# Optimization experiments

Measured on AMD Instinct MI355X. Metric: run time of the kernel, lower is better.

The kernel has to match this reference:

```python
import jax, jax.numpy as jnp
import numpy as np

N = 50000      # nodes
E = 800000     # edges (avg degree 16)
D = 64         # num_node_features
H = 64         # hidden_channels
G = 512        # graphs in batch
OUT = 32       # final linear output
NEG_SLOPE = 0.2


def setup_inputs() -> dict:
    key = jax.random.key(0)
    ks = jax.random.split(key, 20)
    s = 0.1  # param init scale
    inp = {
        "x": jax.random.normal(ks[0], (N, D), jnp.float32),
        "edge_index": jax.random.randint(ks[1], (2, E), 0, N, dtype=jnp.int64),
        "batch": jnp.sort(jax.random.randint(ks[2], (N,), 0, G, dtype=jnp.int64)),
        # GATv2 layer 1 (D -> H)
        "Wl1": jax.random.normal(ks[3], (D, H), jnp.float32) * s,
        "bl1": jnp.zeros((H,), jnp.float32),
        "Wr1": jax.random.normal(ks[4], (D, H), jnp.float32) * s,
        "br1": jnp.zeros((H,), jnp.float32),
        "att1": jax.random.normal(ks[5], (H,), jnp.float32) * s,
        "bias1": jnp.zeros((H,), jnp.float32),
        # GATv2 layer 2 (H -> H)
        "Wl2": jax.random.normal(ks[6], (H, H), jnp.float32) * s,
        "bl2": jnp.zeros((H,), jnp.float32),
        "Wr2": jax.random.normal(ks[7], (H, H), jnp.float32) * s,
        "br2": jnp.zeros((H,), jnp.float32),
        "att2": jax.random.normal(ks[8], (H,), jnp.float32) * s,
        "bias2": jnp.zeros((H,), jnp.float32),
        # final classifier
        "lin_w": jax.random.normal(ks[9], (H, OUT), jnp.float32) * s,
        "lin_b": jnp.zeros((OUT,), jnp.float32),
    }
    return inp


def _gatv2(x, src, dst, Wl, bl, Wr, br, att, bias):
    # GATv2Conv, heads=1, PyG semantics: messages flow src -> dst
    xl = x @ Wl + bl                       # [N, H] source transform (also the message)
    xr = x @ Wr + br                       # [N, H] destination transform
    z = xl[src] + xr[dst]                  # [E, H] gather
    e = jax.nn.leaky_relu(z, NEG_SLOPE) @ att  # [E] edge scores
    # segment softmax over edges grouped by destination node
    m = jax.ops.segment_max(e, dst, num_segments=N)   # [N]
    ex = jnp.exp(e - m[dst])                          # [E]
    denom = jax.ops.segment_sum(ex, dst, num_segments=N)  # [N]
    alpha = ex / denom[dst]                            # [E]
    out = jax.ops.segment_sum(alpha[:, None] * xl[src], dst, num_segments=N)  # [N, H]
    return out + bias


def reference(x, edge_index, batch,
              Wl1, bl1, Wr1, br1, att1, bias1,
              Wl2, bl2, Wr2, br2, att2, bias2,
              lin_w, lin_b):
    src, dst = edge_index[0], edge_index[1]
    h = jax.nn.relu(_gatv2(x, src, dst, Wl1, bl1, Wr1, br1, att1, bias1))
    h = jax.nn.relu(_gatv2(h, src, dst, Wl2, bl2, Wr2, br2, att2, bias2))
    # global mean pool over graphs
    sums = jax.ops.segment_sum(h, batch, num_segments=G)          # [G, H]
    cnts = jax.ops.segment_sum(jnp.ones((h.shape[0],), h.dtype), batch, num_segments=G)
    pooled = sums / jnp.maximum(cnts, 1.0)[:, None]
    # dropout(p=0.5) is identity at inference
    return pooled @ lin_w + lin_b                                  # [G, 32]
```

## Files before the change

kernel.cpp:

```cpp
#include <hip/hip_runtime.h>
#include <hip/hip_fp16.h>
#include <math.h>


#define ELLC    48
#define OVF_CAP 65536
#define ECHUNK  2048

typedef int      vint4 __attribute__((ext_vector_type(4)));
typedef _Float16 half4 __attribute__((ext_vector_type(4)));

#define GROWS 32
template <typename T>
__device__ __forceinline__ void dual_gemm_slim(
    int bid, int t,
    const T* __restrict__ X,
    const float* __restrict__ Wl, const float* __restrict__ bl,
    const float* __restrict__ Wr, const float* __restrict__ br,
    _Float16* __restrict__ xl, float* __restrict__ xr, int n,
    float* xS) {
    int row0 = bid * GROWS;
    for (int i = t; i < GROWS * 16; i += 256) {
        int r = row0 + (i >> 4);
        float4 v = make_float4(0.f, 0.f, 0.f, 0.f);
        if (r < n) {
            if constexpr (sizeof(T) == 2) {
                half4 hv = ((const half4*)(X + (size_t)r * 64))[i & 15];
                v = make_float4((float)hv[0], (float)hv[1], (float)hv[2], (float)hv[3]);
            } else {
                v = ((const float4*)(X + (size_t)r * 64))[i & 15];
            }
        }
        ((float4*)xS)[i] = v;
    }
    __syncthreads();
    int h  = t & 63;
    int rb = t >> 6;
    float accl[8], accr[8];
#pragma unroll
    for (int i = 0; i < 8; ++i) { accl[i] = 0.f; accr[i] = 0.f; }
#pragma unroll 4
    for (int d = 0; d < 64; ++d) {
        float wl = Wl[d * 64 + h];
        float wr = Wr[d * 64 + h];
#pragma unroll
        for (int i = 0; i < 8; ++i) {
            float xv = xS[(rb + 4 * i) * 64 + d];
            accl[i] += xv * wl;
            accr[i] += xv * wr;
        }
    }
    float blv = bl[h], brv = br[h];
#pragma unroll
    for (int i = 0; i < 8; ++i) {
        int r = row0 + rb + 4 * i;
        if (r < n) {
            xl[(size_t)r * 64 + h] = (_Float16)(accl[i] + blv);
            xr[(size_t)r * 64 + h] = accr[i] + brv;
        }
    }
}

__global__ __launch_bounds__(256) void dual_gemm64_f16_kernel(
    const _Float16* __restrict__ X,
    const float* __restrict__ Wl, const float* __restrict__ bl,
    const float* __restrict__ Wr, const float* __restrict__ br,
    _Float16* __restrict__ xl, float* __restrict__ xr, int n) {
    __shared__ float xS[GROWS * 64];
    dual_gemm_slim<_Float16>(blockIdx.x, threadIdx.x, X, Wl, bl, Wr, br,
                             xl, xr, n, xS);
}

__global__ __launch_bounds__(256) void fill_gemm_kernel(
    const int* __restrict__ src, const int* __restrict__ dst,
    int* __restrict__ cnt, unsigned short* __restrict__ ell,
    int* __restrict__ novf, int* __restrict__ ovf_dst, int* __restrict__ ovf_src,
    int E, int N, int psize, int fb, int ggrid,
    const float* __restrict__ X,
    const float* __restrict__ Wl, const float* __restrict__ bl,
    const float* __restrict__ Wr, const float* __restrict__ br,
    _Float16* __restrict__ xl, float* __restrict__ xr) {
    __shared__ float xS[GROWS * 64];
    int b = blockIdx.x;
    int q = b / 24, r = b % 24;
    if (r >= 16) {
        int vg = q * 8 + (r - 16);
        if (vg < ggrid)
            dual_gemm_slim<float>(vg, threadIdx.x, X, Wl, bl, Wr, br,
                                  xl, xr, N, xS);
        return;
    }
    int vb = q * 16 + r;
    if (vb >= fb) return;
    int t     = threadIdx.x;
    int chunk = vb >> 3;
    int p     = vb & 7;
    int d0    = p * psize;
    int d1    = min(N, d0 + psize);
    int e0    = chunk * ECHUNK;
    int e1    = min(E, e0 + ECHUNK);
    int nq    = (e1 - e0) >> 2;
    const vint4* dst4 = (const vint4*)(dst + e0);
    const vint4* src4 = (const vint4*)(src + e0);

    auto scatter4 = [&](vint4 dv, vint4 sv) {
#pragma unroll
        for (int k = 0; k < 4; ++k) {
            int d = dv[k];
            int s = sv[k];
            if (d >= d0 && d < d1) {
                int pos = atomicAdd(&cnt[d], 1);
                if (pos < ELLC) {
                    ell[d * ELLC + pos] = (unsigned short)s;
                } else {
                    int j = atomicAdd(novf, 1);
                    if (j < OVF_CAP) { ovf_dst[j] = d; ovf_src[j] = s; }
                }
            }
        }
    };

    if (nq == (ECHUNK >> 2)) {
        vint4 dvA = __builtin_nontemporal_load(&dst4[t]);
        vint4 svA = __builtin_nontemporal_load(&src4[t]);
        vint4 dvB = __builtin_nontemporal_load(&dst4[t + 256]);
        vint4 svB = __builtin_nontemporal_load(&src4[t + 256]);
        scatter4(dvA, svA);
        scatter4(dvB, svB);
    } else {
        for (int qq = t; qq < nq; qq += 256) {
            vint4 dv = __builtin_nontemporal_load(&dst4[qq]);
            vint4 sv = __builtin_nontemporal_load(&src4[qq]);
            scatter4(dv, sv);
        }
        for (int e = e0 + (nq << 2) + t; e < e1; e += 256) {
            int d = dst[e];
            if (d >= d0 && d < d1) {
                int pos = atomicAdd(&cnt[d], 1);
                int s   = src[e];
                if (pos < ELLC) {
                    ell[d * ELLC + pos] = (unsigned short)s;
                } else {
                    int j = atomicAdd(novf, 1);
                    if (j < OVF_CAP) { ovf_dst[j] = d; ovf_src[j] = s; }
                }
            }
        }
    }
}

__global__ __launch_bounds__(256) void gat_aggregate_kernel(
    const _Float16* __restrict__ xl, const float* __restrict__ xr,
    const int* __restrict__ cnt, const unsigned short* __restrict__ ell,
    const int* __restrict__ novf, const int* __restrict__ ovf_dst,
    const int* __restrict__ ovf_src,
    const float* __restrict__ att, const float* __restrict__ bias,
    _Float16* __restrict__ out, int n) {
    int wid  = (blockIdx.x * blockDim.x + threadIdx.x) >> 6;
    int lane = threadIdx.x & 63;
    if (wid >= n) return;
    int g = lane >> 4;
    int l = lane & 15;
    int d = wid;

    float4 att4 = ((const float4*)att)[l];
    float4 b4   = ((const float4*)bias)[l];
    int deg_d = cnt[d];
    int nd  = min(deg_d, ELLC);
    int beg = d * ELLC;

    float  s   = 0.f;
    float4 acc = make_float4(0.f, 0.f, 0.f, 0.f);

    if (deg_d > 0) {
        int myidx = 0;
        if (lane < ELLC) myidx = (int)ell[beg + lane];
        int i_first = __shfl(myidx, 0);

        float4 xr4 = ((const float4*)(xr + (size_t)d * 64))[l];

#pragma unroll 6
        for (int k = 0; k * 8 < nd; ++k) {
            int  sa = k * 8 + g, sb = sa + 4;
            bool aa = sa < nd,   ab = sb < nd;
            int  i0 = __shfl(myidx, sa); if (!aa) i0 = i_first;
            int  i1 = __shfl(myidx, sb); if (!ab) i1 = i_first;
            half4 h0 = ((const half4*)(xl + (size_t)i0 * 64))[l];
            half4 h1 = ((const half4*)(xl + (size_t)i1 * 64))[l];
            float4 x0 = make_float4((float)h0[0], (float)h0[1], (float)h0[2], (float)h0[3]);
            float4 x1 = make_float4((float)h1[0], (float)h1[1], (float)h1[2], (float)h1[3]);
            float z, c0 = 0.f, c1 = 0.f;
            z = x0.x + xr4.x; c0 += ((z > 0.f) ? z : 0.2f * z) * att4.x;
            z = x0.y + xr4.y; c0 += ((z > 0.f) ? z : 0.2f * z) * att4.y;
            z = x0.z + xr4.z; c0 += ((z > 0.f) ? z : 0.2f * z) * att4.z;
            z = x0.w + xr4.w; c0 += ((z > 0.f) ? z : 0.2f * z) * att4.w;
            z = x1.x + xr4.x; c1 += ((z > 0.f) ? z : 0.2f * z) * att4.x;
            z = x1.y + xr4.y; c1 += ((z > 0.f) ? z : 0.2f * z) * att4.y;
            z = x1.z + xr4.z; c1 += ((z > 0.f) ? z : 0.2f * z) * att4.z;
            z = x1.w + xr4.w; c1 += ((z > 0.f) ? z : 0.2f * z) * att4.w;
#pragma unroll
            for (int sh = 8; sh >= 1; sh >>= 1) {
                c0 += __shfl_xor(c0, sh);
                c1 += __shfl_xor(c1, sh);
            }
            float w0 = aa ? __expf(fminf(c0, 30.f)) : 0.f;
            float w1 = ab ? __expf(fminf(c1, 30.f)) : 0.f;
            s += w0 + w1;
            acc.x += w0 * x0.x + w1 * x1.x;
            acc.y += w0 * x0.y + w1 * x1.y;
            acc.z += w0 * x0.z + w1 * x1.z;
            acc.w += w0 * x0.w + w1 * x1.w;
        }
        if (deg_d > ELLC) {
            int no = min(*novf, OVF_CAP);
            for (int j = g; j < no; j += 4) {
                bool active = (ovf_dst[j] == d);
                int  i0     = active ? ovf_src[j] : i_first;
                half4 h0 = ((const half4*)(xl + (size_t)i0 * 64))[l];
                float4 x0 = make_float4((float)h0[0], (float)h0[1], (float)h0[2], (float)h0[3]);
                float z, c0 = 0.f;
                z = x0.x + xr4.x; c0 += ((z > 0.f) ? z : 0.2f * z) * att4.x;
                z = x0.y + xr4.y; c0 += ((z > 0.f) ? z : 0.2f * z) * att4.y;
                z = x0.z + xr4.z; c0 += ((z > 0.f) ? z : 0.2f * z) * att4.z;
                z = x0.w + xr4.w; c0 += ((z > 0.f) ? z : 0.2f * z) * att4.w;
#pragma unroll
                for (int sh = 8; sh >= 1; sh >>= 1) c0 += __shfl_xor(c0, sh);
                float w0 = active ? __expf(fminf(c0, 30.f)) : 0.f;
                s += w0;
                acc.x += w0 * x0.x;
                acc.y += w0 * x0.y;
                acc.z += w0 * x0.z;
                acc.w += w0 * x0.w;
            }
        }
#pragma unroll
        for (int mask = 16; mask <= 32; mask <<= 1) {
            s     += __shfl_xor(s, mask);
            acc.x += __shfl_xor(acc.x, mask);
            acc.y += __shfl_xor(acc.y, mask);
            acc.z += __shfl_xor(acc.z, mask);
            acc.w += __shfl_xor(acc.w, mask);
        }
    }
    if (g == 0) {
        float inv = (s > 0.f) ? (1.f / s) : 0.f;
        half4 hv;
        hv[0] = (_Float16)fmaxf(acc.x * inv + b4.x, 0.f);
        hv[1] = (_Float16)fmaxf(acc.y * inv + b4.y, 0.f);
        hv[2] = (_Float16)fmaxf(acc.z * inv + b4.z, 0.f);
        hv[3] = (_Float16)fmaxf(acc.w * inv + b4.w, 0.f);
        ((half4*)(out + (size_t)d * 64))[l] = hv;
    }
}

__global__ __launch_bounds__(256) void pool_kernel(
    const _Float16* __restrict__ h, const int* __restrict__ batch,
    float* __restrict__ sums, float* __restrict__ cnts, int n, int nwaves) {
    int wid  = (blockIdx.x * blockDim.x + threadIdx.x) >> 6;
    int lane = threadIdx.x & 63;
    int per   = (n + nwaves - 1) / nwaves;
    int start = wid * per;
    int end   = min(n, start + per);
    if (start >= end) return;
    int cur   = batch[start];
    float acc = 0.f, cnt = 0.f;
    for (int i = start; i < end; ++i) {
        int g = batch[i];
        if (g != cur) {
            atomicAdd(&sums[cur * 64 + lane], acc);
            if (lane == 0) atomicAdd(&cnts[cur], cnt);
            acc = 0.f; cnt = 0.f; cur = g;
        }
        acc += (float)h[(size_t)i * 64 + lane];
        cnt += 1.f;
    }
    atomicAdd(&sums[cur * 64 + lane], acc);
    if (lane == 0) atomicAdd(&cnts[cur], cnt);
}

__global__ __launch_bounds__(256) void final_kernel(
    const float* __restrict__ sums, const float* __restrict__ cnts,
    const float* __restrict__ lin_w, const float* __restrict__ lin_b,
    float* __restrict__ out, int total) {
    int tid = blockIdx.x * blockDim.x + threadIdx.x;
    if (tid >= total) return;
    int g = tid >> 5, o = tid & 31;
    float inv = 1.f / fmaxf(cnts[g], 1.f);
    float a = 0.f;
    for (int h = 0; h < 64; ++h) a += sums[g * 64 + h] * lin_w[h * 32 + o];
    out[tid] = a * inv + lin_b[o];
}

extern "C" void kernel_launch(void* const* d_in, const int* in_sizes, int n_in,
                              void* d_out, int out_size, void* d_ws, size_t ws_size,
                              hipStream_t stream) {
    const float* x     = (const float*)d_in[0];
    const int*   ei    = (const int*)d_in[1];
    const int*   batch = (const int*)d_in[2];
    const float* Wl1   = (const float*)d_in[3];
    const float* bl1   = (const float*)d_in[4];
    const float* Wr1   = (const float*)d_in[5];
    const float* br1   = (const float*)d_in[6];
    const float* att1  = (const float*)d_in[7];
    const float* bias1 = (const float*)d_in[8];
    const float* Wl2   = (const float*)d_in[9];
    const float* bl2   = (const float*)d_in[10];
    const float* Wr2   = (const float*)d_in[11];
    const float* br2   = (const float*)d_in[12];
    const float* att2  = (const float*)d_in[13];
    const float* bias2 = (const float*)d_in[14];
    const float* lin_w = (const float*)d_in[15];
    const float* lin_b = (const float*)d_in[16];
    float* out = (float*)d_out;

    const int N = in_sizes[0] / 64;
    const int E = in_sizes[1] / 2;
    const int G = out_size / 32;
    const int* src = ei;
    const int* dst = ei + E;

    char*  ws  = (char*)d_ws;
    size_t off = 0;
    auto alloc = [&](size_t bytes) -> void* {
        void* p = ws + off;
        off += bytes;
        off = (off + 255) & ~(size_t)255;
        return p;
    };
    _Float16* xl   = (_Float16*)alloc((size_t)N * 64 * sizeof(_Float16));
    float* xr      = (float*)alloc((size_t)N * 64 * sizeof(float));
    _Float16* h1   = (_Float16*)alloc((size_t)N * 64 * sizeof(_Float16));
    int*   cnt     = (int*)alloc((size_t)N * sizeof(int));
    int*   novf    = (int*)alloc(256);
    float* sums    = (float*)alloc((size_t)G * 64 * sizeof(float));
    float* cnts    = (float*)alloc((size_t)G * sizeof(float));
    char*  zend    = ws + off;
    unsigned short* ell = (unsigned short*)alloc((size_t)N * ELLC * sizeof(unsigned short));
    int*   ovf_dst = (int*)alloc((size_t)OVF_CAP * sizeof(int));
    int*   ovf_src = (int*)alloc((size_t)OVF_CAP * sizeof(int));

    (void)hipMemsetAsync(cnt, 0, (size_t)(zend - (char*)cnt), stream);

    int ggrid  = (N + GROWS - 1) / GROWS;
    int agrid  = (N + 3) / 4;
    int nchunk = (E + ECHUNK - 1) / ECHUNK;
    int fb     = nchunk * 8;
    int psize  = (N + 7) / 8;
    int ngroups = max((fb + 15) / 16, (ggrid + 7) / 8);
    int igrid   = ngroups * 24;

    fill_gemm_kernel<<<igrid, 256, 0, stream>>>(
        src, dst, cnt, ell, novf, ovf_dst, ovf_src, E, N, psize, fb, ggrid,
        x, Wl1, bl1, Wr1, br1, xl, xr);

    gat_aggregate_kernel<<<agrid, 256, 0, stream>>>(
        xl, xr, cnt, ell, novf, ovf_dst, ovf_src, att1, bias1, h1, N);

    dual_gemm64_f16_kernel<<<ggrid, 256, 0, stream>>>(
        h1, Wl2, bl2, Wr2, br2, xl, xr, N);

    gat_aggregate_kernel<<<agrid, 256, 0, stream>>>(
        xl, xr, cnt, ell, novf, ovf_dst, ovf_src, att2, bias2, h1, N);

    const int NWAVES = 2048;
    pool_kernel<<<512, 256, 0, stream>>>(h1, batch, sums, cnts, N, NWAVES);
    int total = G * 32;
    final_kernel<<<(total + 255) / 256, 256, 0, stream>>>(sums, cnts, lin_w, lin_b, out, total);
}
```

Measured before the change: 248.1 us.

## Fuse mean-pool and final linear into one per-graph kernel using binary search

Replaces the atomic-based pooling kernel and the separate classifier kernel with a single kernel that launches one block per graph. Each block binary-searches the sorted batch array for its node range, reduces features in shared memory, divides by the count and applies the linear layer. This removes one launch, the global atomics and the sums/cnts workspace and its memset. It relies on batch being sorted and may load-balance poorly if graph sizes vary.

```diff
diff --git a/kernel.cpp b/kernel.cpp
--- a/kernel.cpp
+++ b/kernel.cpp
@@ -253,42 +253,41 @@
     }
 }
 
-__global__ __launch_bounds__(256) void pool_kernel(
+__global__ __launch_bounds__(256) void pool_final_kernel(
     const _Float16* __restrict__ h, const int* __restrict__ batch,
-    float* __restrict__ sums, float* __restrict__ cnts, int n, int nwaves) {
-    int wid  = (blockIdx.x * blockDim.x + threadIdx.x) >> 6;
-    int lane = threadIdx.x & 63;
-    int per   = (n + nwaves - 1) / nwaves;
-    int start = wid * per;
-    int end   = min(n, start + per);
-    if (start >= end) return;
-    int cur   = batch[start];
-    float acc = 0.f, cnt = 0.f;
-    for (int i = start; i < end; ++i) {
-        int g = batch[i];
-        if (g != cur) {
-            atomicAdd(&sums[cur * 64 + lane], acc);
-            if (lane == 0) atomicAdd(&cnts[cur], cnt);
-            acc = 0.f; cnt = 0.f; cur = g;
-        }
-        acc += (float)h[(size_t)i * 64 + lane];
-        cnt += 1.f;
-    }
-    atomicAdd(&sums[cur * 64 + lane], acc);
-    if (lane == 0) atomicAdd(&cnts[cur], cnt);
-}
-
-__global__ __launch_bounds__(256) void final_kernel(
-    const float* __restrict__ sums, const float* __restrict__ cnts,
     const float* __restrict__ lin_w, const float* __restrict__ lin_b,
-    float* __restrict__ out, int total) {
-    int tid = blockIdx.x * blockDim.x + threadIdx.x;
-    if (tid >= total) return;
-    int g = tid >> 5, o = tid & 31;
-    float inv = 1.f / fmaxf(cnts[g], 1.f);
-    float a = 0.f;
-    for (int h = 0; h < 64; ++h) a += sums[g * 64 + h] * lin_w[h * 32 + o];
-    out[tid] = a * inv + lin_b[o];
+    float* __restrict__ out, int N, int G) {
+    int g = blockIdx.x;
+    int t = threadIdx.x;
+    auto lb = [&](int key) {
+        int lo = 0, hi = N;
+        while (lo < hi) {
+            int mid = (lo + hi) >> 1;
+            if (batch[mid] < key) lo = mid + 1; else hi = mid;
+        }
+        return lo;
+    };
+    int start = lb(g), end = lb(g + 1);
+
+    __shared__ float part[4][64];
+    __shared__ float pooled[64];
+    int f = t & 63, w = t >> 6;
+    float acc = 0.f;
+    for (int i = start + w; i < end; i += 4)
+        acc += (float)h[(size_t)i * 64 + f];
+    part[w][f] = acc;
+    __syncthreads();
+    if (t < 64) {
+        float s = part[0][t] + part[1][t] + part[2][t] + part[3][t];
+        pooled[t] = s / fmaxf((float)(end - start), 1.f);
+    }
+    __syncthreads();
+    if (t < 32) {
+        float a = 0.f;
+#pragma unroll 8
+        for (int hh = 0; hh < 64; ++hh) a += pooled[hh] * lin_w[hh * 32 + t];
+        out[g * 32 + t] = a + lin_b[t];
+    }
 }
 
 extern "C" void kernel_launch(void* const* d_in, const int* in_sizes, int n_in,
@@ -332,8 +331,6 @@
     _Float16* h1   = (_Float16*)alloc((size_t)N * 64 * sizeof(_Float16));
     int*   cnt     = (int*)alloc((size_t)N * sizeof(int));
     int*   novf    = (int*)alloc(256);
-    float* sums    = (float*)alloc((size_t)G * 64 * sizeof(float));
-    float* cnts    = (float*)alloc((size_t)G * sizeof(float));
     char*  zend    = ws + off;
     unsigned short* ell = (unsigned short*)alloc((size_t)N * ELLC * sizeof(unsigned short));
     int*   ovf_dst = (int*)alloc((size_t)OVF_CAP * sizeof(int));
@@ -362,8 +359,5 @@
     gat_aggregate_kernel<<<agrid, 256, 0, stream>>>(
         xl, xr, cnt, ell, novf, ovf_dst, ovf_src, att2, bias2, h1, N);
 
-    const int NWAVES = 2048;
-    pool_kernel<<<512, 256, 0, stream>>>(h1, batch, sums, cnts, N, NWAVES);
-    int total = G * 32;
-    final_kernel<<<(total + 255) / 256, 256, 0, stream>>>(sums, cnts, lin_w, lin_b, out, total);
-}
+    pool_final_kernel<<<G, 256, 0, stream>>>(h1, batch, lin_w, lin_b, out, N, G);
+}
```

Measured after the change: 243.4 us. About the same (-1.9%).
